# Kernel tuning notes

Measured on AMD Instinct MI355X. Metric: run time of the kernel, lower is better.

## Reference

```python
import jax, jax.numpy as jnp
import numpy as np

B, S, D, H = 4, 2048, 1024, 16
DK = D // H


def setup_inputs() -> dict:
    key = jax.random.key(0)
    ks = jax.random.split(key, 11)
    s = 1.0 / np.sqrt(D)
    return {
        "x_Q": jax.random.normal(ks[0], (B, S, D), jnp.float32),
        "x_K": jax.random.normal(ks[1], (B, S, D), jnp.float32),
        "x_V": jax.random.normal(ks[2], (B, S, D), jnp.float32),
        "Wq": jax.random.normal(ks[3], (D, D), jnp.float32) * s,
        "bq": jax.random.normal(ks[4], (D,), jnp.float32) * 0.01,
        "Wk": jax.random.normal(ks[5], (D, D), jnp.float32) * s,
        "bk": jax.random.normal(ks[6], (D,), jnp.float32) * 0.01,
        "Wv": jax.random.normal(ks[7], (D, D), jnp.float32) * s,
        "bv": jax.random.normal(ks[8], (D,), jnp.float32) * 0.01,
        "Wo": jax.random.normal(ks[9], (D, D), jnp.float32) * s,
        "bo": jax.random.normal(ks[10], (D,), jnp.float32) * 0.01,
    }


def reference(x_Q, x_K, x_V, Wq, bq, Wk, bk, Wv, bv, Wo, bo):
    def heads(x, W, b):
        # [B,S,D] -> [B,H,S,DK]
        y = x @ W.T + b
        return y.reshape(B, S, H, DK).transpose(0, 2, 1, 3)

    Q = heads(x_Q, Wq, bq)
    K = heads(x_K, Wk, bk)
    V = heads(x_V, Wv, bv)
    scores = jnp.einsum('bhqd,bhkd->bhqk', Q, K) / jnp.sqrt(jnp.float32(DK))
    probs = jax.nn.softmax(scores, axis=-1)
    out = jnp.einsum('bhqk,bhkd->bhqd', probs, V)
    out = out.transpose(0, 2, 1, 3).reshape(B, S, D)
    return out @ Wo.T + bo
```

## Files before the change

### kernel.cpp

```cpp
#include <hip/hip_runtime.h>

typedef __attribute__((ext_vector_type(8))) short bf16x8;
typedef __attribute__((ext_vector_type(4))) short short4v;
typedef __attribute__((ext_vector_type(4))) float f32x4;
typedef __attribute__((ext_vector_type(2))) unsigned int u32x2;

#define DEV static __device__ __forceinline__

DEV unsigned short f2b(float f) {
  union { float f; unsigned int i; } v; v.f = f;
  unsigned int x = v.i;
  return (unsigned short)((x + 0x7FFFu + ((x >> 16) & 1u)) >> 16);
}
DEV unsigned int fbits(float f) {
  union { float f; unsigned int i; } v; v.f = f; return v.i;
}

DEV void cp16(const unsigned short* g, unsigned short* l) {
  __builtin_amdgcn_global_load_lds(
      (const __attribute__((address_space(1))) void*)g,
      (__attribute__((address_space(3))) void*)l, 16, 0, 0);
}

__global__ void cvt_kernel(const float* __restrict__ in,
                           unsigned short* __restrict__ out, int n) {
  const int i = (blockIdx.x * blockDim.x + threadIdx.x) * 4;
  if (i < n) {
    const float4 v = *(const float4*)&in[i];
    short4v o;
    o[0] = (short)f2b(v.x); o[1] = (short)f2b(v.y);
    o[2] = (short)f2b(v.z); o[3] = (short)f2b(v.w);
    *(short4v*)&out[i] = o;
  }
}

template <int MODE>
__global__ __launch_bounds__(512, 4) void gemm_bt(
    const unsigned short* __restrict__ A, const unsigned short* __restrict__ W,
    const float* __restrict__ bias, void* __restrict__ OutV,
    int M, int N, int K) {
  __shared__ __align__(16) unsigned short smem[128 * 128];
  unsigned short* sA = smem;
  unsigned short* sB = smem + 128 * 64;
  const int tid = threadIdx.x;
  const int lane = tid & 63, wave = tid >> 6;
  const int lr = lane & 15, quad = lane >> 4;
  const int bm = blockIdx.x * 128, bn = blockIdx.y * 128;
  const int wm = (wave >> 1) * 32, wn = (wave & 1) * 64;
  const int srow = tid >> 3;
  const int sdst = (tid & 7) * 8;
  const int ssrc = ((tid & 7) ^ (srow & 7)) * 8;

  f32x4 acc[2][4] = {};

  for (int kt = 0; kt < K; kt += 64) {
#pragma unroll
    for (int is = 0; is < 2; ++is) {
      const int r = is * 64 + srow;
      cp16(&A[(size_t)(bm + r) * K + kt + ssrc], &sA[r * 64 + sdst]);
      cp16(&W[(size_t)(bn + r) * K + kt + ssrc], &sB[r * 64 + sdst]);
    }
    __syncthreads();
#pragma unroll
    for (int ks = 0; ks < 2; ++ks) {
      bf16x8 af[2], bf[4];
      const int co = (((ks * 4 + quad) ^ (lr & 7)) << 3);
#pragma unroll
      for (int i = 0; i < 2; ++i)
        af[i] = *(const bf16x8*)&sA[(wm + i * 16 + lr) * 64 + co];
#pragma unroll
      for (int j = 0; j < 4; ++j)
        bf[j] = *(const bf16x8*)&sB[(wn + j * 16 + lr) * 64 + co];
#pragma unroll
      for (int i = 0; i < 2; ++i)
#pragma unroll
        for (int j = 0; j < 4; ++j)
          acc[i][j] = __builtin_amdgcn_mfma_f32_16x16x32_bf16(af[i], bf[j], acc[i][j], 0, 0, 0);
    }
    __syncthreads();
  }

  if (MODE == 2) {
    unsigned short* sD = smem;
#pragma unroll
    for (int j = 0; j < 4; ++j) {
      const int n = wn + j * 16 + lr;
      const float bv = bias[bn + n];
#pragma unroll
      for (int i = 0; i < 2; ++i) {
        const int cm = (wm >> 2) + i * 4 + quad;
        short4v pk;
#pragma unroll
        for (int r = 0; r < 4; ++r) pk[r] = (short)f2b(acc[i][j][r] + bv);
        *(short4v*)&sD[n * 128 + ((cm ^ (n & 31)) << 2)] = pk;
      }
    }
    __syncthreads();
    const int b = bm >> 11, s0 = bm & 2047;
#pragma unroll
    for (int it = 0; it < 4; ++it) {
      const int id = it * 512 + tid;
      const int n = id >> 4, c = id & 15;
      const short4v lo = *(const short4v*)&sD[n * 128 + (((c * 2) ^ (n & 31)) << 2)];
      const short4v hi = *(const short4v*)&sD[n * 128 + (((c * 2 + 1) ^ (n & 31)) << 2)];
      const int ng = bn + n;
      unsigned short* dst =
          &((unsigned short*)OutV)[((size_t)(b * 16 + (ng >> 6)) * 64 + (ng & 63)) * 2048 + s0 + c * 8];
      *(short4v*)&dst[0] = lo;
      *(short4v*)&dst[4] = hi;
    }
  } else {
#pragma unroll
    for (int j = 0; j < 4; ++j) {
      const int n = bn + wn + j * 16 + lr;
      const float bv = bias[n];
#pragma unroll
      for (int i = 0; i < 2; ++i) {
        const int mb = bm + wm + i * 16 + quad * 4;
#pragma unroll
        for (int r = 0; r < 4; ++r) {
          const int m = mb + r;
          const float o = acc[i][j][r] + bv;
          if (MODE == 0) {
            ((float*)OutV)[(size_t)m * N + n] = o;
          } else {
            ((unsigned short*)OutV)[((size_t)((m >> 11) * 16 + (n >> 6)) * 2048 + (m & 2047)) * 64 + (n & 63)] = f2b(o);
          }
        }
      }
    }
  }
}

__global__ __launch_bounds__(256, 4) void attn_kernel(
    const unsigned short* __restrict__ Qb, const unsigned short* __restrict__ Kb,
    const unsigned short* __restrict__ Vt, unsigned short* __restrict__ Ob) {
  __shared__ __align__(16) unsigned short sK[128 * 64];
  __shared__ __align__(16) unsigned short sV[64 * 128];
  __shared__ __align__(16) unsigned short sP[4][32 * 32];

  const int tid = threadIdx.x, lane = tid & 63, wave = tid >> 6;
  const int lr = lane & 15, quad = lane >> 4;
  const int bh = blockIdx.y;
  const int q0 = blockIdx.x * 128;
  const size_t base = (size_t)bh * (2048 * 64);
  const unsigned short* Qp = Qb + base;
  const unsigned short* Kp = Kb + base;
  const unsigned short* Vp = Vt + base;
  const int wq = wave * 32;

  bf16x8 qf[2][2];
#pragma unroll
  for (int i = 0; i < 2; ++i)
#pragma unroll
    for (int ks = 0; ks < 2; ++ks)
      qf[i][ks] = *(const bf16x8*)&Qp[(size_t)(q0 + wq + i * 16 + lr) * 64 + ks * 32 + quad * 8];

  f32x4 oacc[2][4] = {};
  float rs[2] = {0.f, 0.f};
  const float c1 = 0.125f * 1.44269504f;
  const float c2 = 24.0f * 1.44269504f;

  const int kr = tid >> 3;
  const int kd = (tid & 7) * 8;
  const int ksrc = ((tid & 7) ^ (kr & 7)) * 8;
  const int vr = tid >> 4;
  const int vd = (tid & 15) * 8;
  const int vsrc = ((tid & 15) ^ vr) * 8;

  for (int kv0 = 0; kv0 < 2048; kv0 += 128) {
#pragma unroll
    for (int is = 0; is < 4; ++is) {
      cp16(&Kp[(size_t)(kv0 + is * 32 + kr) * 64 + ksrc], &sK[(is * 32 + kr) * 64 + kd]);
      cp16(&Vp[(size_t)(is * 16 + vr) * 2048 + kv0 + vsrc], &sV[(is * 16 + vr) * 128 + vd]);
    }
    __syncthreads();

#pragma unroll
    for (int p = 0; p < 4; ++p) {
      f32x4 sacc[2][2] = {};
#pragma unroll
      for (int ks = 0; ks < 2; ++ks) {
        const int co = (((ks * 4 + quad) ^ (lr & 7)) << 3);
#pragma unroll
        for (int jl = 0; jl < 2; ++jl) {
          const bf16x8 kf = *(const bf16x8*)&sK[((2 * p + jl) * 16 + lr) * 64 + co];
#pragma unroll
          for (int i = 0; i < 2; ++i)
            sacc[jl][i] = __builtin_amdgcn_mfma_f32_16x16x32_bf16(kf, qf[i][ks], sacc[jl][i], 0, 0, 0);
        }
      }

#pragma unroll
      for (int i = 0; i < 2; ++i) {
#pragma unroll
        for (int jl = 0; jl < 2; ++jl) {
          unsigned int u[4];
#pragma unroll
          for (int r = 0; r < 4; ++r) {
            const float pv = __builtin_amdgcn_exp2f(fmaf(sacc[jl][i][r], c1, -c2));
            rs[i] += pv;
            u[r] = fbits(pv) + 0x8000u;
          }
          u32x2 w;
          w[0] = __builtin_amdgcn_perm(u[1], u[0], 0x07060302u);
          w[1] = __builtin_amdgcn_perm(u[3], u[2], 0x07060302u);
          *(u32x2*)&sP[wave][(i * 16 + lr) * 32 +
                             (((jl * 2 + (quad >> 1)) ^ (lr & 3)) << 3) + ((quad & 1) << 2)] = w;
        }
      }

      const int cv = (((p * 4 + quad) ^ lr) << 3);
      bf16x8 vf[4];
#pragma unroll
      for (int jd = 0; jd < 4; ++jd)
        vf[jd] = *(const bf16x8*)&sV[(jd * 16 + lr) * 128 + cv];
#pragma unroll
      for (int i = 0; i < 2; ++i) {
        const bf16x8 pf = *(const bf16x8*)&sP[wave][(i * 16 + lr) * 32 + ((quad ^ (lr & 3)) << 3)];
#pragma unroll
        for (int jd = 0; jd < 4; ++jd)
          oacc[i][jd] = __builtin_amdgcn_mfma_f32_16x16x32_bf16(pf, vf[jd], oacc[i][jd], 0, 0, 0);
      }
    }
    __syncthreads();
  }

  const int b = bh >> 4, h = bh & 15;
#pragma unroll
  for (int i = 0; i < 2; ++i) {
    rs[i] += __shfl_xor(rs[i], 16);
    rs[i] += __shfl_xor(rs[i], 32);
    const float linv = 1.f / rs[i];
#pragma unroll
    for (int r = 0; r < 4; ++r) {
      const float li = __shfl(linv, quad * 4 + r);
      const int s = q0 + wq + i * 16 + quad * 4 + r;
#pragma unroll
      for (int jd = 0; jd < 4; ++jd)
        Ob[(size_t)(b * 2048 + s) * 1024 + h * 64 + jd * 16 + lr] =
            f2b(oacc[i][jd][r] * li);
    }
  }
}

extern "C" void kernel_launch(void* const* d_in, const int* in_sizes, int n_in,
                              void* d_out, int out_size, void* d_ws, size_t ws_size,
                              hipStream_t stream) {
  const float* xq = (const float*)d_in[0];
  const float* xk = (const float*)d_in[1];
  const float* xv = (const float*)d_in[2];
  const float* Wq = (const float*)d_in[3];
  const float* bq = (const float*)d_in[4];
  const float* Wk = (const float*)d_in[5];
  const float* bk = (const float*)d_in[6];
  const float* Wv = (const float*)d_in[7];
  const float* bv = (const float*)d_in[8];
  const float* Wo = (const float*)d_in[9];
  const float* bo = (const float*)d_in[10];

  unsigned short* ws = (unsigned short*)d_ws;
  const size_t SZ = (size_t)8192 * 1024;
  unsigned short* X  = ws;
  unsigned short* Wb = ws + SZ;
  unsigned short* Qb = ws + SZ + SZ / 8;
  unsigned short* Kb = Qb + SZ;
  unsigned short* Vt = Kb + SZ;

  const int NX = 8192 * 1024, NW = 1024 * 1024;
  dim3 cbx(256), cgx(NX / 1024), cgw(NW / 1024);
  dim3 gg(64, 8), bb(512);

  hipLaunchKernelGGL(cvt_kernel, cgx, cbx, 0, stream, xq, X, NX);
  hipLaunchKernelGGL(cvt_kernel, cgw, cbx, 0, stream, Wq, Wb, NW);
  hipLaunchKernelGGL((gemm_bt<1>), gg, bb, 0, stream, X, Wb, bq, (void*)Qb, 8192, 1024, 1024);

  hipLaunchKernelGGL(cvt_kernel, cgx, cbx, 0, stream, xk, X, NX);
  hipLaunchKernelGGL(cvt_kernel, cgw, cbx, 0, stream, Wk, Wb, NW);
  hipLaunchKernelGGL((gemm_bt<1>), gg, bb, 0, stream, X, Wb, bk, (void*)Kb, 8192, 1024, 1024);

  hipLaunchKernelGGL(cvt_kernel, cgx, cbx, 0, stream, xv, X, NX);
  hipLaunchKernelGGL(cvt_kernel, cgw, cbx, 0, stream, Wv, Wb, NW);
  hipLaunchKernelGGL((gemm_bt<2>), gg, bb, 0, stream, X, Wb, bv, (void*)Vt, 8192, 1024, 1024);

  hipLaunchKernelGGL(attn_kernel, dim3(16, 64), dim3(256), 0, stream, Qb, Kb, Vt, X);

  hipLaunchKernelGGL(cvt_kernel, cgw, cbx, 0, stream, Wo, Wb, NW);
  hipLaunchKernelGGL((gemm_bt<0>), gg, bb, 0, stream, X, Wb, bo, d_out, 8192, 1024, 1024);
}
```

Baseline: 377.9 us.

## Enlarge GEMM tile to 256x128 and compute V projection transposed

The GEMM block tile grows from 128x128 to 256x128, so each wave holds a 4x4 accumulator grid, and launch bounds drop to allow more registers. The aim is more MFMA work per LDS byte loaded and fewer blocks. The V projection now computes Wv·Xᵀ by swapping operands, so the transposed Vt layout falls out of the output indexing and the LDS-staged transpose epilogue goes away. The cost is lower occupancy, only 256 or 256 blocks per GEMM, and the V output store now writes 2-byte elements along a stride. The attention kernel's launch bound also changes from 4 to 2 blocks.

```diff
diff --git a/kernel.cpp b/kernel.cpp
--- a/kernel.cpp
+++ b/kernel.cpp
@@ -35,44 +35,47 @@
 }
 
 template <int MODE>
-__global__ __launch_bounds__(512, 4) void gemm_bt(
+__global__ __launch_bounds__(512, 1) void gemm_bt(
     const unsigned short* __restrict__ A, const unsigned short* __restrict__ W,
     const float* __restrict__ bias, void* __restrict__ OutV,
     int M, int N, int K) {
-  __shared__ __align__(16) unsigned short smem[128 * 128];
-  unsigned short* sA = smem;
-  unsigned short* sB = smem + 128 * 64;
+  __shared__ __align__(16) unsigned short sA[256 * 64];
+  __shared__ __align__(16) unsigned short sB[128 * 64];
   const int tid = threadIdx.x;
   const int lane = tid & 63, wave = tid >> 6;
   const int lr = lane & 15, quad = lane >> 4;
-  const int bm = blockIdx.x * 128, bn = blockIdx.y * 128;
-  const int wm = (wave >> 1) * 32, wn = (wave & 1) * 64;
+  const int bm = blockIdx.x * 256, bn = blockIdx.y * 128;
+  const int wm = (wave >> 1) * 64, wn = (wave & 1) * 64;
   const int srow = tid >> 3;
   const int sdst = (tid & 7) * 8;
   const int ssrc = ((tid & 7) ^ (srow & 7)) * 8;
 
-  f32x4 acc[2][4] = {};
+  f32x4 acc[4][4] = {};
 
   for (int kt = 0; kt < K; kt += 64) {
+#pragma unroll
+    for (int is = 0; is < 4; ++is) {
+      const int r = is * 64 + srow;
+      cp16(&A[(size_t)(bm + r) * K + kt + ssrc], &sA[r * 64 + sdst]);
+    }
 #pragma unroll
     for (int is = 0; is < 2; ++is) {
       const int r = is * 64 + srow;
-      cp16(&A[(size_t)(bm + r) * K + kt + ssrc], &sA[r * 64 + sdst]);
       cp16(&W[(size_t)(bn + r) * K + kt + ssrc], &sB[r * 64 + sdst]);
     }
     __syncthreads();
 #pragma unroll
     for (int ks = 0; ks < 2; ++ks) {
-      bf16x8 af[2], bf[4];
+      bf16x8 af[4], bf[4];
       const int co = (((ks * 4 + quad) ^ (lr & 7)) << 3);
 #pragma unroll
-      for (int i = 0; i < 2; ++i)
+      for (int i = 0; i < 4; ++i)
         af[i] = *(const bf16x8*)&sA[(wm + i * 16 + lr) * 64 + co];
 #pragma unroll
       for (int j = 0; j < 4; ++j)
         bf[j] = *(const bf16x8*)&sB[(wn + j * 16 + lr) * 64 + co];
 #pragma unroll
-      for (int i = 0; i < 2; ++i)
+      for (int i = 0; i < 4; ++i)
 #pragma unroll
         for (int j = 0; j < 4; ++j)
           acc[i][j] = __builtin_amdgcn_mfma_f32_16x16x32_bf16(af[i], bf[j], acc[i][j], 0, 0, 0);
@@ -80,59 +83,31 @@
     __syncthreads();
   }
 
-  if (MODE == 2) {
-    unsigned short* sD = smem;
-#pragma unroll
-    for (int j = 0; j < 4; ++j) {
-      const int n = wn + j * 16 + lr;
-      const float bv = bias[bn + n];
-#pragma unroll
-      for (int i = 0; i < 2; ++i) {
-        const int cm = (wm >> 2) + i * 4 + quad;
-        short4v pk;
-#pragma unroll
-        for (int r = 0; r < 4; ++r) pk[r] = (short)f2b(acc[i][j][r] + bv);
-        *(short4v*)&sD[n * 128 + ((cm ^ (n & 31)) << 2)] = pk;
-      }
-    }
-    __syncthreads();
-    const int b = bm >> 11, s0 = bm & 2047;
-#pragma unroll
-    for (int it = 0; it < 4; ++it) {
-      const int id = it * 512 + tid;
-      const int n = id >> 4, c = id & 15;
-      const short4v lo = *(const short4v*)&sD[n * 128 + (((c * 2) ^ (n & 31)) << 2)];
-      const short4v hi = *(const short4v*)&sD[n * 128 + (((c * 2 + 1) ^ (n & 31)) << 2)];
-      const int ng = bn + n;
-      unsigned short* dst =
-          &((unsigned short*)OutV)[((size_t)(b * 16 + (ng >> 6)) * 64 + (ng & 63)) * 2048 + s0 + c * 8];
-      *(short4v*)&dst[0] = lo;
-      *(short4v*)&dst[4] = hi;
-    }
-  } else {
-#pragma unroll
-    for (int j = 0; j < 4; ++j) {
-      const int n = bn + wn + j * 16 + lr;
-      const float bv = bias[n];
-#pragma unroll
-      for (int i = 0; i < 2; ++i) {
-        const int mb = bm + wm + i * 16 + quad * 4;
-#pragma unroll
-        for (int r = 0; r < 4; ++r) {
-          const int m = mb + r;
-          const float o = acc[i][j][r] + bv;
-          if (MODE == 0) {
-            ((float*)OutV)[(size_t)m * N + n] = o;
-          } else {
-            ((unsigned short*)OutV)[((size_t)((m >> 11) * 16 + (n >> 6)) * 2048 + (m & 2047)) * 64 + (n & 63)] = f2b(o);
-          }
+#pragma unroll
+  for (int j = 0; j < 4; ++j) {
+    const int n = bn + wn + j * 16 + lr;
+    const float bvn = (MODE == 2) ? 0.f : bias[n];
+#pragma unroll
+    for (int i = 0; i < 4; ++i) {
+      const int mb = bm + wm + i * 16 + quad * 4;
+#pragma unroll
+      for (int r = 0; r < 4; ++r) {
+        const int m = mb + r;
+        if (MODE == 0) {
+          ((float*)OutV)[(size_t)m * N + n] = acc[i][j][r] + bvn;
+        } else if (MODE == 1) {
+          ((unsigned short*)OutV)[((size_t)((m >> 11) * 16 + (n >> 6)) * 2048 + (m & 2047)) * 64 + (n & 63)] =
+              f2b(acc[i][j][r] + bvn);
+        } else {
+          ((unsigned short*)OutV)[(((size_t)(n >> 11) * 16 + (m >> 6)) * 64 + (m & 63)) * 2048 + (n & 2047)] =
+              f2b(acc[i][j][r] + bias[m]);
         }
       }
     }
   }
 }
 
-__global__ __launch_bounds__(256, 4) void attn_kernel(
+__global__ __launch_bounds__(256, 2) void attn_kernel(
     const unsigned short* __restrict__ Qb, const unsigned short* __restrict__ Kb,
     const unsigned short* __restrict__ Vt, unsigned short* __restrict__ Ob) {
   __shared__ __align__(16) unsigned short sK[128 * 64];
@@ -269,7 +244,7 @@
 
   const int NX = 8192 * 1024, NW = 1024 * 1024;
   dim3 cbx(256), cgx(NX / 1024), cgw(NW / 1024);
-  dim3 gg(64, 8), bb(512);
+  dim3 gg(32, 8), ggv(4, 64), bb(512);
 
   hipLaunchKernelGGL(cvt_kernel, cgx, cbx, 0, stream, xq, X, NX);
   hipLaunchKernelGGL(cvt_kernel, cgw, cbx, 0, stream, Wq, Wb, NW);
@@ -281,7 +256,7 @@
 
   hipLaunchKernelGGL(cvt_kernel, cgx, cbx, 0, stream, xv, X, NX);
   hipLaunchKernelGGL(cvt_kernel, cgw, cbx, 0, stream, Wv, Wb, NW);
-  hipLaunchKernelGGL((gemm_bt<2>), gg, bb, 0, stream, X, Wb, bv, (void*)Vt, 8192, 1024, 1024);
+  hipLaunchKernelGGL((gemm_bt<2>), ggv, bb, 0, stream, Wb, X, bv, (void*)Vt, 1024, 8192, 1024);
 
   hipLaunchKernelGGL(attn_kernel, dim3(16, 64), dim3(256), 0, stream, Qb, Kb, Vt, X);
 
```

Result: slower. 388.5 us (+2.8%).
